# Performance work log

Measured on AMD Instinct MI355X. Metric: run time of the kernel, lower is better.

## Reference

```python
import jax, jax.numpy as jnp
import numpy as np

DIM = 128
HEADS = 8
DIM_HEAD = 128  # must equal DIM for the module's shapes to be consistent
INNER = HEADS * DIM_HEAD  # 1024
B, N = 16, 2048
SCALE = 1.0 / (DIM // 2 + 1)  # 1/65


def setup_inputs() -> dict:
    key = jax.random.key(0)
    k1, k2, k3 = jax.random.split(key, 3)
    x = jax.random.normal(k1, (B, N, DIM), dtype=jnp.float32)
    w_qkv = jax.random.normal(k2, (DIM, 3 * INNER), dtype=jnp.float32) * (DIM ** -0.5)
    w_out = jax.random.normal(k3, (INNER, DIM), dtype=jnp.float32) * (INNER ** -0.5)
    b_out = jnp.zeros((DIM,), dtype=jnp.float32)
    return {"x": x, "w_qkv": w_qkv, "w_out": w_out, "b_out": b_out}


def reference(x, w_qkv, w_out, b_out):
    b, n, dim = x.shape
    qkv = x @ w_qkv                                   # [b, n, 3*inner]
    q, k, v = jnp.split(qkv, 3, axis=-1)
    # b n (h d) -> b h n d
    to_heads = lambda t: t.reshape(b, n, HEADS, DIM_HEAD).transpose(0, 2, 1, 3)
    q, k, v = to_heads(q), to_heads(k), to_heads(v)
    xq_ft = jnp.abs(jnp.fft.rfft(q * SCALE, axis=-1))  # [b, h, n, f] real
    xk_ft = jnp.abs(jnp.fft.rfft(k * SCALE, axis=-1))
    xv_ft = jnp.fft.rfft(v, axis=-1)                   # complex
    att = jnp.einsum('bhex,bhey->bhxy', xq_ft, xk_ft)  # [b, h, f, f]
    att = jax.nn.softmax(att, axis=-1)
    xqkv_ft = jnp.einsum('bhxy,bhey->bhex', att.astype(xv_ft.dtype), xv_ft)
    out = jnp.fft.irfft(xqkv_ft, n=dim, axis=-1)       # [b, h, n, dim]
    out = out.transpose(0, 2, 1, 3).reshape(b, n, HEADS * dim)  # b n (h d)
    return out @ w_out + b_out
```

## Files before the change

### kernel.cpp

```cpp
#include <hip/hip_runtime.h>
#include <hip/hip_bf16.h>
#include <math.h>

#define NB    16
#define NSEQ  2048
#define MROWS (NB*NSEQ)
#define QKT_ROWS 1088

typedef __attribute__((ext_vector_type(8))) short bf16x8;
typedef __attribute__((ext_vector_type(4))) float f32x4;

__device__ __forceinline__ void g2l16(const void* g, void* l) {
    __builtin_amdgcn_global_load_lds(
        (const __attribute__((address_space(1))) void*)g,
        (__attribute__((address_space(3))) void*)l, 16, 0, 0);
}

__device__ __forceinline__ ushort f2bfu(float x) {
    __hip_bfloat16 t = __float2bfloat16(x);
    return *reinterpret_cast<ushort*>(&t);
}

__global__ __launch_bounds__(256) void k_misc(const float* __restrict__ x,
                                              const float* __restrict__ wqkv,
                                              const float* __restrict__ wout,
                                              __hip_bfloat16* __restrict__ Xb,
                                              ushort* __restrict__ Wvb,
                                              ushort* __restrict__ Wqkb,
                                              ushort* __restrict__ Gcat,
                                              ushort* __restrict__ Fcs,
                                              ushort* __restrict__ Bas) {
    __shared__ float tc[128], ts[128];
    int tid = threadIdx.x;
    int bid = blockIdx.x;
    if (bid < 4096) {
        int i = bid * 256 + tid;
        float4 v = ((const float4*)x)[i];
        __hip_bfloat16 o[4] = {__float2bfloat16(v.x), __float2bfloat16(v.y),
                               __float2bfloat16(v.z), __float2bfloat16(v.w)};
        *(ushort4*)((ushort*)Xb + (size_t)i * 4) = *(const ushort4*)o;
    } else if (bid < 4224) {
        int u = bid - 4096;
        float4 v = *(const float4*)(wqkv + (size_t)u * 3072 + 2048 + tid * 4);
        ushort o[4] = {f2bfu(v.x), f2bfu(v.y), f2bfu(v.z), f2bfu(v.w)};
        *(ushort4*)(Wvb + (size_t)u * 1024 + tid * 4) = *(const ushort4*)o;
    } else if (bid < 4352) {
        int u = bid - 4224;
        #pragma unroll
        for (int it = 0; it < 2; ++it) {
            int i = it * 256 + tid;
            float4 v = ((const float4*)(wqkv + (size_t)u * 3072))[i];
            ushort o[4] = {f2bfu(v.x), f2bfu(v.y), f2bfu(v.z), f2bfu(v.w)};
            *(ushort4*)(Wqkb + (size_t)u * 2048 + i * 4) = *(const ushort4*)o;
        }
    } else if (bid < 4872) {
        int hx = bid - 4352;
        if (tid < 128) {
            float a = (float)tid / 64.0f;
            tc[tid] = cospif(a);
            ts[tid] = sinpif(a);
        }
        __syncthreads();
        if (tid < 128) {
            int h = hx / 65, xx = hx - h * 65;
            float w = (xx == 0 || xx == 64) ? (1.0f / 128.0f) : (2.0f / 128.0f);
            float ar = 0.f, ai = 0.f;
            #pragma unroll 8
            for (int d = 0; d < 128; ++d) {
                float wv = wout[(size_t)(h * 128 + d) * 128 + tid];
                int m = (xx * d) & 127;
                ar = fmaf(wv, tc[m], ar);
                ai = fmaf(wv, ts[m], ai);
            }
            ushort* gp = Gcat + ((size_t)(h * 128 + tid)) * 160;
            gp[xx] = f2bfu(ar * w);
            gp[80 + xx] = f2bfu(-ai * w);
            if (xx == 0) {
                for (int k = 65; k < 80; ++k) gp[k] = 0;
                for (int k = 145; k < 160; ++k) gp[k] = 0;
            }
        }
    } else if (bid < 4888) {
        int r = (bid - 4872) * 16 + (tid >> 4);
        int d = r & 127;
        int y0 = (tid & 15) * 6;
        #pragma unroll
        for (int k = 0; k < 6; ++k) {
            int y = y0 + k;
            float v = 0.f;
            if (y < 65) {
                float a = (float)((d * y) & 127) / 64.0f;
                v = (r < 128) ? cospif(a) : -sinpif(a);
            }
            Fcs[r * 96 + y] = f2bfu(v);
        }
    } else {
        int idx = bid - 4888;
        int rj = idx * 16 + (tid >> 4);
        int ri = (rj >= 80) ? 1 : 0;
        int f = rj - ri * 80;
        int d0 = (tid & 15) * 8;
        #pragma unroll
        for (int k = 0; k < 8; ++k) {
            int d = d0 + k;
            float a = (float)((f * d) & 127) / 64.0f;
            float v = (ri ? -sinpif(a) : cospif(a)) * (1.0f / 65.0f);
            Bas[rj * 128 + d] = f2bfu(v);
        }
    }
}

__global__ __launch_bounds__(256) void k_wfold(const ushort* __restrict__ Wqkb,
                                               const ushort* __restrict__ Bas,
                                               ushort* __restrict__ Wt2) {
    __shared__ ushort As[128 * 128];
    __shared__ ushort Bs[160 * 128];
    int tid = threadIdx.x;
    int wave = tid >> 6, lane = tid & 63;
    int reg = blockIdx.x >> 3, h = blockIdx.x & 7;
    const ushort* ga = Wqkb + reg * 1024 + h * 128;
    #pragma unroll
    for (int it = 0; it < 8; ++it) {
        int q0 = wave * 512 + it * 64;
        int q = q0 + lane;
        int row = q >> 4, cp = q & 15;
        int gc = cp ^ (row & 15);
        g2l16(ga + (size_t)row * 2048 + gc * 8, As + q0 * 8);
    }
    #pragma unroll
    for (int it = 0; it < 10; ++it) {
        int q0 = it * 256 + wave * 64;
        int q = q0 + lane;
        int row = q >> 4, cp = q & 15;
        int gc = cp ^ (row & 15);
        g2l16(Bas + (size_t)row * 128 + gc * 8, Bs + q0 * 8);
    }
    __syncthreads();

    f32x4 acc[4][5];
    #pragma unroll
    for (int i = 0; i < 4; ++i)
        #pragma unroll
        for (int j = 0; j < 5; ++j) acc[i][j] = (f32x4){0.f, 0.f, 0.f, 0.f};

    int lr = lane & 15, lk = lane >> 4;
    int wr = (wave >> 1) * 64;
    int wn = (wave & 1) * 80;
    #pragma unroll
    for (int kk = 0; kk < 4; ++kk) {
        bf16x8 af[4], bfr[5];
        int c = kk * 4 + lk;
        #pragma unroll
        for (int i = 0; i < 4; ++i) {
            int m = wr + i * 16 + lr;
            af[i] = *(const bf16x8*)(As + m * 128 + (c ^ (m & 15)) * 8);
        }
        #pragma unroll
        for (int j = 0; j < 5; ++j) {
            int n = wn + j * 16 + lr;
            bfr[j] = *(const bf16x8*)(Bs + n * 128 + (c ^ (n & 15)) * 8);
        }
        #pragma unroll
        for (int i = 0; i < 4; ++i)
            #pragma unroll
            for (int j = 0; j < 5; ++j)
                acc[i][j] = __builtin_amdgcn_mfma_f32_16x16x32_bf16(af[i], bfr[j], acc[i][j], 0, 0, 0);
    }

    #pragma unroll
    for (int j = 0; j < 5; ++j) {
        int rj = wn + j * 16 + lr;
        int n = (h * 2 + reg) * 160 + rj;
        #pragma unroll
        for (int i = 0; i < 4; ++i) {
            int c0 = wr + i * 16 + lk * 4;
            union { ushort4 u4; ushort u[4]; } pk;
            #pragma unroll
            for (int r = 0; r < 4; ++r) pk.u[r] = f2bfu(acc[i][j][r]);
            *(ushort4*)(Wt2 + (size_t)n * 128 + c0) = pk.u4;
        }
    }
}

__global__ __launch_bounds__(256, 1) void k_fuse(const __hip_bfloat16* __restrict__ Xb,
                                                 const ushort* __restrict__ Wt2,
                                                 float* __restrict__ attp) {
    __shared__ ushort Bs[320 * 128];
    __shared__ ushort As[128 * 128];
    __shared__ ushort S[160 * 128];
    int tid = threadIdx.x;
    int wave = tid >> 6, lane = tid & 63;
    int lr = lane & 15, lk = lane >> 4;
    int lin = blockIdx.y * 128 + blockIdx.x;
    int nl = (lin & 7) * 128 + (lin >> 3);
    int b = nl >> 6;
    int rem = nl & 63;
    int h = rem >> 3, ech = rem & 7;
    size_t erow0 = (size_t)b * NSEQ + (size_t)ech * 256;

    const ushort* wh = Wt2 + (size_t)h * 320 * 128;
    #pragma unroll
    for (int it = 0; it < 20; ++it) {
        int q0 = it * 256 + wave * 64;
        int q = q0 + lane;
        int row = q >> 4, cp = q & 15;
        int gc = cp ^ (row & 15);
        g2l16(wh + (size_t)row * 128 + gc * 8, Bs + q0 * 8);
    }
    {
        const ushort* gx = (const ushort*)Xb + erow0 * 128;
        #pragma unroll
        for (int it = 0; it < 8; ++it) {
            int q0 = wave * 512 + it * 64;
            int q = q0 + lane;
            int row = q >> 4, cp = q & 15;
            int gc = cp ^ (row & 15);
            g2l16(gx + (size_t)row * 128 + gc * 8, As + q0 * 8);
        }
    }
    __syncthreads();

    f32x4 acc2a[5], acc2b[5];
    #pragma unroll
    for (int j = 0; j < 5; ++j) {
        acc2a[j] = (f32x4){0.f, 0.f, 0.f, 0.f};
        acc2b[j] = (f32x4){0.f, 0.f, 0.f, 0.f};
    }

    int esl = wave * 32;
    #pragma unroll
    for (int et = 0; et < 2; ++et) {
        f32x4 acc1[20][2];
        #pragma unroll
        for (int nt = 0; nt < 20; ++nt)
            #pragma unroll
            for (int ei = 0; ei < 2; ++ei) acc1[nt][ei] = (f32x4){0.f, 0.f, 0.f, 0.f};
        #pragma unroll
        for (int ks = 0; ks < 4; ++ks) {
            int c = ks * 4 + lk;
            bf16x8 xa[2];
            #pragma unroll
            for (int ei = 0; ei < 2; ++ei) {
                int m = esl + ei * 16 + lr;
                xa[ei] = *(const bf16x8*)(As + m * 128 + (c ^ (m & 15)) * 8);
            }
            #pragma unroll
            for (int nt = 0; nt < 20; ++nt) {
                int n = nt * 16 + lr;
                bf16x8 wb = *(const bf16x8*)(Bs + n * 128 + (c ^ (n & 15)) * 8);
                #pragma unroll
                for (int ei = 0; ei < 2; ++ei)
                    acc1[nt][ei] = __builtin_amdgcn_mfma_f32_16x16x32_bf16(xa[ei], wb, acc1[nt][ei], 0, 0, 0);
            }
        }
        #pragma unroll
        for (int grp = 0; grp < 2; ++grp) {
            #pragma unroll
            for (int t = 0; t < 5; ++t) {
                int srow = grp * 80 + t * 16 + lr;
                int sw = (srow & 7) << 3;
                #pragma unroll
                for (int ei = 0; ei < 2; ++ei) {
                    f32x4 re = acc1[grp * 10 + t][ei];
                    f32x4 im = acc1[grp * 10 + t + 5][ei];
                    union { ushort4 u4; ushort u[4]; } pk;
                    #pragma unroll
                    for (int r = 0; r < 4; ++r)
                        pk.u[r] = f2bfu(__builtin_amdgcn_sqrtf(re[r] * re[r] + im[r] * im[r]));
                    int e4 = (esl + ei * 16 + lk * 4) ^ sw;
                    *(ushort4*)(S + srow * 128 + e4) = pk.u4;
                }
            }
        }
        __syncthreads();
        if (et == 0) {
            const ushort* gx = (const ushort*)Xb + (erow0 + 128) * 128;
            #pragma unroll
            for (int it = 0; it < 8; ++it) {
                int q0 = wave * 512 + it * 64;
                int q = q0 + lane;
                int row = q >> 4, cp = q & 15;
                int gc = cp ^ (row & 15);
                g2l16(gx + (size_t)row * 128 + gc * 8, As + q0 * 8);
            }
        }
        #pragma unroll
        for (int ks = 0; ks < 4; ++ks) {
            int cg = ks * 4 + lk;
            int xr = wave * 16 + lr;
            bf16x8 qa = *(const bf16x8*)(S + xr * 128 + ((cg ^ (xr & 7)) * 8));
            bf16x8 qb;
            if (wave == 0) {
                int xr2 = 64 + lr;
                qb = *(const bf16x8*)(S + xr2 * 128 + ((cg ^ (xr2 & 7)) * 8));
            }
            #pragma unroll
            for (int ty = 0; ty < 5; ++ty) {
                int yr = 80 + ty * 16 + lr;
                bf16x8 kb = *(const bf16x8*)(S + yr * 128 + ((cg ^ (yr & 7)) * 8));
                acc2a[ty] = __builtin_amdgcn_mfma_f32_16x16x32_bf16(qa, kb, acc2a[ty], 0, 0, 0);
                if (wave == 0)
                    acc2b[ty] = __builtin_amdgcn_mfma_f32_16x16x32_bf16(qb, kb, acc2b[ty], 0, 0, 0);
            }
        }
        if (et == 0) __syncthreads();
    }

    float* outp = attp + ((size_t)(b * 8 + h) * 8 + ech) * 6400;
    #pragma unroll
    for (int ty = 0; ty < 5; ++ty) {
        #pragma unroll
        for (int r = 0; r < 4; ++r) {
            outp[(wave * 16 + lk * 4 + r) * 80 + ty * 16 + lr] = acc2a[ty][r];
            if (wave == 0)
                outp[(64 + lk * 4 + r) * 80 + ty * 16 + lr] = acc2b[ty][r];
        }
    }
}

__global__ void k_softmax(const float* __restrict__ attp, ushort* __restrict__ AttB) {
    int xx = blockIdx.x;
    int bh = blockIdx.y;
    int lane = threadIdx.x;
    ushort* Ab = AttB + (size_t)bh * 8320;
    if (xx >= 65) {
        Ab[xx * 104 + lane] = 0;
        if (lane < 40) Ab[xx * 104 + 64 + lane] = 0;
        return;
    }
    const float* base = attp + (size_t)bh * 8 * 6400 + xx * 80;
    float v0 = 0.f, v1 = 0.f;
    #pragma unroll
    for (int c = 0; c < 8; ++c) {
        v0 += base[(size_t)c * 6400 + lane];
        if (lane == 0) v1 += base[(size_t)c * 6400 + 64];
    }
    float v1b = __shfl(v1, 0);
    float m = fmaxf(v0, v1b);
    #pragma unroll
    for (int off = 32; off >= 1; off >>= 1) m = fmaxf(m, __shfl_xor(m, off));
    float e0 = expf(v0 - m);
    float e1 = expf(v1b - m);
    float s = e0;
    #pragma unroll
    for (int off = 32; off >= 1; off >>= 1) s += __shfl_xor(s, off);
    s += e1;
    float inv = 1.0f / s;
    Ab[xx * 104 + lane] = f2bfu(e0 * inv);
    if (lane == 0) Ab[xx * 104 + 64] = f2bfu(e1 * inv);
    if (lane < 39) Ab[xx * 104 + 65 + lane] = 0;
}

__global__ __launch_bounds__(256) void k_TP(const ushort* __restrict__ AttB,
                                            const ushort* __restrict__ Fcs,
                                            const ushort* __restrict__ Gcat,
                                            ushort* __restrict__ Pt) {
    __shared__ ushort A3[128 * 168];
    int tid = threadIdx.x;
    int wave = tid >> 6, lane = tid & 63;
    int lr = lane & 15, quad = lane >> 4;
    int chalf = blockIdx.x, bh = blockIdx.y;
    int b = bh >> 3, h = bh & 7;

    uint2 z2; z2.x = 0; z2.y = 0;
    uint2* A3v = (uint2*)A3;
    #pragma unroll 4
    for (int i = tid; i < 128 * 168 / 4; i += 256) A3v[i] = z2;
    __syncthreads();
    const ushort* Ab = AttB + (size_t)bh * 8320;

    f32x4 acc1[4][5];
    #pragma unroll
    for (int i = 0; i < 4; ++i)
        #pragma unroll
        for (int j = 0; j < 5; ++j) acc1[i][j] = (f32x4){0.f, 0.f, 0.f, 0.f};
    #pragma unroll
    for (int ks = 0; ks < 3; ++ks) {
        bf16x8 af[4], bfr[5];
        #pragma unroll
        for (int mi = 0; mi < 4; ++mi)
            af[mi] = *(const bf16x8*)(Fcs + (size_t)((wave * 4 + mi) * 16 + lr) * 96 + ks * 32 + quad * 8);
        #pragma unroll
        for (int nt = 0; nt < 5; ++nt)
            bfr[nt] = *(const bf16x8*)(Ab + (nt * 16 + lr) * 104 + ks * 32 + quad * 8);
        #pragma unroll
        for (int mi = 0; mi < 4; ++mi)
            #pragma unroll
            for (int nt = 0; nt < 5; ++nt)
                acc1[mi][nt] = __builtin_amdgcn_mfma_f32_16x16x32_bf16(af[mi], bfr[nt], acc1[mi][nt], 0, 0, 0);
    }
    #pragma unroll
    for (int nt = 0; nt < 5; ++nt) {
        int x = nt * 16 + lr;
        if (x < 65) {
            #pragma unroll
            for (int mi = 0; mi < 4; ++mi) {
                int wbase = (wave * 4 + mi) * 16 + quad * 4;
                #pragma unroll
                for (int r = 0; r < 4; ++r) {
                    int which = wbase + r;
                    int d = which & 127;
                    int kc = (which >> 7) * 80 + x;
                    A3[d * 168 + kc] = f2bfu(acc1[mi][nt][r]);
                }
            }
        }
    }
    __syncthreads();

    f32x4 acc2[2][4];
    #pragma unroll
    for (int i = 0; i < 2; ++i)
        #pragma unroll
        for (int j = 0; j < 4; ++j) acc2[i][j] = (f32x4){0.f, 0.f, 0.f, 0.f};
    const ushort* Gh = Gcat + (size_t)h * 128 * 160;
    #pragma unroll
    for (int ks = 0; ks < 5; ++ks) {
        bf16x8 a2[2], b2[4];
        #pragma unroll
        for (int mi = 0; mi < 2; ++mi)
            a2[mi] = *(const bf16x8*)(A3 + ((wave * 2 + mi) * 16 + lr) * 168 + ks * 32 + quad * 8);
        #pragma unroll
        for (int nt = 0; nt < 4; ++nt)
            b2[nt] = *(const bf16x8*)(Gh + (size_t)(chalf * 64 + nt * 16 + lr) * 160 + ks * 32 + quad * 8);
        #pragma unroll
        for (int mi = 0; mi < 2; ++mi)
            #pragma unroll
            for (int nt = 0; nt < 4; ++nt)
                acc2[mi][nt] = __builtin_amdgcn_mfma_f32_16x16x32_bf16(a2[mi], b2[nt], acc2[mi][nt], 0, 0, 0);
    }
    #pragma unroll
    for (int mi = 0; mi < 2; ++mi) {
        int dbase = (wave * 2 + mi) * 16 + quad * 4;
        #pragma unroll
        for (int nt = 0; nt < 4; ++nt) {
            int c = chalf * 64 + nt * 16 + lr;
            union { ushort4 u4; ushort u[4]; } pk;
            #pragma unroll
            for (int r = 0; r < 4; ++r) pk.u[r] = f2bfu(acc2[mi][nt][r]);
            *(ushort4*)(Pt + ((size_t)(b * 128 + c)) * 1024 + h * 128 + dbase) = pk.u4;
        }
    }
}

__global__ __launch_bounds__(256) void k_R(const ushort* __restrict__ Wvb,
                                           const ushort* __restrict__ Pt,
                                           ushort* __restrict__ Rt) {
    __shared__ ushort As[128 * 128];
    __shared__ ushort Bs[128 * 128];
    int tid = threadIdx.x;
    int wave = tid >> 6, lane = tid & 63;
    int b = blockIdx.x;
    const ushort* pb = Pt + (size_t)b * 128 * 1024;

    f32x4 acc[4][4];
    #pragma unroll
    for (int i = 0; i < 4; ++i)
        #pragma unroll
        for (int j = 0; j < 4; ++j) acc[i][j] = (f32x4){0.f, 0.f, 0.f, 0.f};

    int lr = lane & 15, lk = lane >> 4;
    int wr = (wave >> 1) * 64, wc = (wave & 1) * 64;

    for (int k0 = 0; k0 < 1024; k0 += 128) {
        __syncthreads();
        #pragma unroll
        for (int it = 0; it < 8; ++it) {
            int q = wave * 512 + it * 64 + lane;
            int row = q >> 4, cp = q & 15;
            int gc = cp ^ (row & 15);
            int lbase = (wave * 512 + it * 64) * 8;
            g2l16(Wvb + (size_t)row * 1024 + k0 + gc * 8, As + lbase);
            g2l16(pb + (size_t)row * 1024 + k0 + gc * 8, Bs + lbase);
        }
        __syncthreads();
        #pragma unroll
        for (int kk = 0; kk < 4; ++kk) {
            bf16x8 af[4], bfr[4];
            int c = kk * 4 + lk;
            #pragma unroll
            for (int i = 0; i < 4; ++i) {
                int m = wr + i * 16 + lr;
                af[i] = *(const bf16x8*)(As + m * 128 + (c ^ (m & 15)) * 8);
                int n = wc + i * 16 + lr;
                bfr[i] = *(const bf16x8*)(Bs + n * 128 + (c ^ (n & 15)) * 8);
            }
            #pragma unroll
            for (int i = 0; i < 4; ++i)
                #pragma unroll
                for (int j = 0; j < 4; ++j)
                    acc[i][j] = __builtin_amdgcn_mfma_f32_16x16x32_bf16(af[i], bfr[j], acc[i][j], 0, 0, 0);
        }
    }
    #pragma unroll
    for (int i = 0; i < 4; ++i) {
        int ubase = wr + i * 16 + lk * 4;
        #pragma unroll
        for (int j = 0; j < 4; ++j) {
            int n = wc + j * 16 + lr;
            union { ushort4 u4; ushort u[4]; } pk;
            #pragma unroll
            for (int r = 0; r < 4; ++r) pk.u[r] = f2bfu(acc[i][j][r]);
            *(ushort4*)(Rt + (size_t)b * 16384 + n * 128 + ubase) = pk.u4;
        }
    }
}

__global__ __launch_bounds__(256) void k_out(const __hip_bfloat16* __restrict__ Xb,
                                             const ushort* __restrict__ Rt,
                                             const float* __restrict__ bout,
                                             float* __restrict__ out) {
    __shared__ ushort As[128 * 128];
    __shared__ ushort Bs[128 * 128];
    int tid = threadIdx.x;
    int wave = tid >> 6, lane = tid & 63;
    int m0 = blockIdx.x * 128;
    int b = blockIdx.x >> 4;
    const ushort* ga = (const ushort*)Xb + (size_t)m0 * 128;
    const ushort* gb = Rt + (size_t)b * 16384;
    #pragma unroll
    for (int it = 0; it < 8; ++it) {
        int q = wave * 512 + it * 64 + lane;
        int row = q >> 4, cp = q & 15;
        int gc = cp ^ (row & 15);
        int lbase = (wave * 512 + it * 64) * 8;
        g2l16(ga + (size_t)row * 128 + gc * 8, As + lbase);
        g2l16(gb + (size_t)row * 128 + gc * 8, Bs + lbase);
    }
    __syncthreads();

    f32x4 acc[4][4];
    #pragma unroll
    for (int i = 0; i < 4; ++i)
        #pragma unroll
        for (int j = 0; j < 4; ++j) acc[i][j] = (f32x4){0.f, 0.f, 0.f, 0.f};

    int lr = lane & 15, lk = lane >> 4;
    int wr = (wave >> 1) * 64, wc = (wave & 1) * 64;
    #pragma unroll
    for (int kk = 0; kk < 4; ++kk) {
        bf16x8 af[4], bfr[4];
        int c = kk * 4 + lk;
        #pragma unroll
        for (int i = 0; i < 4; ++i) {
            int m = wr + i * 16 + lr;
            af[i] = *(const bf16x8*)(As + m * 128 + (c ^ (m & 15)) * 8);
            int n = wc + i * 16 + lr;
            bfr[i] = *(const bf16x8*)(Bs + n * 128 + (c ^ (n & 15)) * 8);
        }
        #pragma unroll
        for (int i = 0; i < 4; ++i)
            #pragma unroll
            for (int j = 0; j < 4; ++j)
                acc[i][j] = __builtin_amdgcn_mfma_f32_16x16x32_bf16(af[i], bfr[j], acc[i][j], 0, 0, 0);
    }

    #pragma unroll
    for (int i = 0; i < 4; ++i) {
        int gr = m0 + wr + i * 16 + lk * 4;
        #pragma unroll
        for (int j = 0; j < 4; ++j) {
            int gcol = wc + j * 16 + lr;
            float bias = bout[gcol];
            #pragma unroll
            for (int r = 0; r < 4; ++r)
                out[(size_t)(gr + r) * 128 + gcol] = acc[i][j][r] + bias;
        }
    }
}

extern "C" void kernel_launch(void* const* d_in, const int* in_sizes, int n_in,
                              void* d_out, int out_size, void* d_ws, size_t ws_size,
                              hipStream_t stream) {
    const float* x    = (const float*)d_in[0];
    const float* wqkv = (const float*)d_in[1];
    const float* wout = (const float*)d_in[2];
    const float* bout = (const float*)d_in[3];
    float* out = (float*)d_out;

    char* ws = (char*)d_ws;
    size_t off = 0;
    auto alloc = [&](size_t bytes) -> void* {
        void* p = (void*)(ws + off);
        off += (bytes + 255) & ~(size_t)255;
        return p;
    };
    ushort* Wt2  = (ushort*)alloc((size_t)8 * 320 * 128 * 2);
    ushort* Gcat = (ushort*)alloc((size_t)8 * 128 * 160 * 2);
    ushort* Fcs  = (ushort*)alloc((size_t)256 * 96 * 2);
    ushort* Wvb  = (ushort*)alloc((size_t)128 * 1024 * 2);
    ushort* Wqkb = (ushort*)alloc((size_t)128 * 2048 * 2);
    ushort* Bas  = (ushort*)alloc((size_t)160 * 128 * 2);
    __hip_bfloat16* Xb = (__hip_bfloat16*)alloc((size_t)MROWS * 128 * 2);
    float* attp = (float*)alloc((size_t)128 * 8 * 6400 * 4);
    ushort* AttB = (ushort*)alloc((size_t)128 * 8320 * 2);
    ushort* Pt  = (ushort*)alloc((size_t)16 * 128 * 1024 * 2);
    ushort* Rt  = (ushort*)alloc((size_t)16 * 128 * 128 * 2);

    k_misc<<<dim3(4898), 256, 0, stream>>>(x, wqkv, wout, Xb, Wvb, Wqkb, Gcat, Fcs, Bas);
    k_wfold<<<dim3(16), 256, 0, stream>>>(Wqkb, Bas, Wt2);
    k_fuse<<<dim3(128, 8), 256, 0, stream>>>(Xb, Wt2, attp);
    k_softmax<<<dim3(80, 128), 64, 0, stream>>>(attp, AttB);
    k_TP<<<dim3(2, 128), 256, 0, stream>>>(AttB, Fcs, Gcat, Pt);
    k_R<<<dim3(16), 256, 0, stream>>>(Wvb, Pt, Rt);
    k_out<<<dim3(256), 256, 0, stream>>>(Xb, Rt, bout, out);
}
```

Before: 171.0 us.

## Restructure fused QK-spectrum kernel with register-resident weights and larger sequence chunks

```diff
diff --git a/kernel.cpp b/kernel.cpp
--- a/kernel.cpp
+++ b/kernel.cpp
@@ -5,7 +5,6 @@
 #define NB    16
 #define NSEQ  2048
 #define MROWS (NB*NSEQ)
-#define QKT_ROWS 1088
 
 typedef __attribute__((ext_vector_type(8))) short bf16x8;
 typedef __attribute__((ext_vector_type(4))) float f32x4;
@@ -182,37 +181,34 @@
     }
 }
 
-__global__ __launch_bounds__(256, 1) void k_fuse(const __hip_bfloat16* __restrict__ Xb,
+__global__ __launch_bounds__(320, 3) void k_fuse(const __hip_bfloat16* __restrict__ Xb,
                                                  const ushort* __restrict__ Wt2,
                                                  float* __restrict__ attp) {
-    __shared__ ushort Bs[320 * 128];
     __shared__ ushort As[128 * 128];
     __shared__ ushort S[160 * 128];
     int tid = threadIdx.x;
     int wave = tid >> 6, lane = tid & 63;
     int lr = lane & 15, lk = lane >> 4;
     int lin = blockIdx.y * 128 + blockIdx.x;
-    int nl = (lin & 7) * 128 + (lin >> 3);
-    int b = nl >> 6;
-    int rem = nl & 63;
-    int h = rem >> 3, ech = rem & 7;
-    size_t erow0 = (size_t)b * NSEQ + (size_t)ech * 256;
-
+    int nl = (lin & 7) * 64 + (lin >> 3);
+    int b = nl >> 5;
+    int epart = (nl >> 3) & 3, h = nl & 7;
+    size_t erow0 = (size_t)b * NSEQ + (size_t)epart * 512;
     const ushort* wh = Wt2 + (size_t)h * 320 * 128;
-    #pragma unroll
-    for (int it = 0; it < 20; ++it) {
-        int q0 = it * 256 + wave * 64;
-        int q = q0 + lane;
-        int row = q >> 4, cp = q & 15;
-        int gc = cp ^ (row & 15);
-        g2l16(wh + (size_t)row * 128 + gc * 8, Bs + q0 * 8);
-    }
+
+    bf16x8 bw[4][4];
+    #pragma unroll
+    for (int ks = 0; ks < 4; ++ks)
+        #pragma unroll
+        for (int rb = 0; rb < 4; ++rb) {
+            int n = rb * 80 + wave * 16 + lr;
+            bw[ks][rb] = *(const bf16x8*)(wh + (size_t)n * 128 + (ks * 4 + lk) * 8);
+        }
+
     {
         const ushort* gx = (const ushort*)Xb + erow0 * 128;
-        #pragma unroll
-        for (int it = 0; it < 8; ++it) {
-            int q0 = wave * 512 + it * 64;
-            int q = q0 + lane;
+        for (int r = wave; r < 32; r += 5) {
+            int q0 = r * 64, q = q0 + lane;
             int row = q >> 4, cp = q & 15;
             int gc = cp ^ (row & 15);
             g2l16(gx + (size_t)row * 128 + gc * 8, As + q0 * 8);
@@ -220,65 +216,42 @@
     }
     __syncthreads();
 
-    f32x4 acc2a[5], acc2b[5];
-    #pragma unroll
-    for (int j = 0; j < 5; ++j) {
-        acc2a[j] = (f32x4){0.f, 0.f, 0.f, 0.f};
-        acc2b[j] = (f32x4){0.f, 0.f, 0.f, 0.f};
-    }
-
-    int esl = wave * 32;
-    #pragma unroll
-    for (int et = 0; et < 2; ++et) {
-        f32x4 acc1[20][2];
-        #pragma unroll
-        for (int nt = 0; nt < 20; ++nt)
-            #pragma unroll
-            for (int ei = 0; ei < 2; ++ei) acc1[nt][ei] = (f32x4){0.f, 0.f, 0.f, 0.f};
-        #pragma unroll
-        for (int ks = 0; ks < 4; ++ks) {
-            int c = ks * 4 + lk;
-            bf16x8 xa[2];
-            #pragma unroll
-            for (int ei = 0; ei < 2; ++ei) {
-                int m = esl + ei * 16 + lr;
-                xa[ei] = *(const bf16x8*)(As + m * 128 + (c ^ (m & 15)) * 8);
-            }
-            #pragma unroll
-            for (int nt = 0; nt < 20; ++nt) {
-                int n = nt * 16 + lr;
-                bf16x8 wb = *(const bf16x8*)(Bs + n * 128 + (c ^ (n & 15)) * 8);
+    f32x4 acc2[5];
+    #pragma unroll
+    for (int j = 0; j < 5; ++j) acc2[j] = (f32x4){0.f, 0.f, 0.f, 0.f};
+
+    for (int it = 0; it < 4; ++it) {
+        #pragma unroll
+        for (int et = 0; et < 8; ++et) {
+            f32x4 a4[4];
+            #pragma unroll
+            for (int rb = 0; rb < 4; ++rb) a4[rb] = (f32x4){0.f, 0.f, 0.f, 0.f};
+            #pragma unroll
+            for (int ks = 0; ks < 4; ++ks) {
+                int m = et * 16 + lr;
+                bf16x8 xa = *(const bf16x8*)(As + m * 128 + (((ks * 4 + lk) ^ (m & 15))) * 8);
                 #pragma unroll
-                for (int ei = 0; ei < 2; ++ei)
-                    acc1[nt][ei] = __builtin_amdgcn_mfma_f32_16x16x32_bf16(xa[ei], wb, acc1[nt][ei], 0, 0, 0);
-            }
-        }
-        #pragma unroll
-        for (int grp = 0; grp < 2; ++grp) {
-            #pragma unroll
-            for (int t = 0; t < 5; ++t) {
-                int srow = grp * 80 + t * 16 + lr;
-                int sw = (srow & 7) << 3;
-                #pragma unroll
-                for (int ei = 0; ei < 2; ++ei) {
-                    f32x4 re = acc1[grp * 10 + t][ei];
-                    f32x4 im = acc1[grp * 10 + t + 5][ei];
-                    union { ushort4 u4; ushort u[4]; } pk;
-                    #pragma unroll
-                    for (int r = 0; r < 4; ++r)
-                        pk.u[r] = f2bfu(__builtin_amdgcn_sqrtf(re[r] * re[r] + im[r] * im[r]));
-                    int e4 = (esl + ei * 16 + lk * 4) ^ sw;
-                    *(ushort4*)(S + srow * 128 + e4) = pk.u4;
-                }
-            }
+                for (int rb = 0; rb < 4; ++rb)
+                    a4[rb] = __builtin_amdgcn_mfma_f32_16x16x32_bf16(xa, bw[ks][rb], a4[rb], 0, 0, 0);
+            }
+            int e4 = et * 16 + lk * 4;
+            int cq = e4 >> 3, sub = e4 & 7;
+            union { ushort4 u4; ushort u[4]; } pq, pk2;
+            #pragma unroll
+            for (int r = 0; r < 4; ++r) {
+                pq.u[r]  = f2bfu(__builtin_amdgcn_sqrtf(a4[0][r] * a4[0][r] + a4[1][r] * a4[1][r]));
+                pk2.u[r] = f2bfu(__builtin_amdgcn_sqrtf(a4[2][r] * a4[2][r] + a4[3][r] * a4[3][r]));
+            }
+            int fq = wave * 16 + lr;
+            int fk = 80 + wave * 16 + lr;
+            *(ushort4*)(S + fq * 128 + ((cq ^ (fq & 15)) << 3) + sub) = pq.u4;
+            *(ushort4*)(S + fk * 128 + ((cq ^ (fk & 15)) << 3) + sub) = pk2.u4;
         }
         __syncthreads();
-        if (et == 0) {
-            const ushort* gx = (const ushort*)Xb + (erow0 + 128) * 128;
-            #pragma unroll
-            for (int it = 0; it < 8; ++it) {
-                int q0 = wave * 512 + it * 64;
-                int q = q0 + lane;
+        if (it < 3) {
+            const ushort* gx = (const ushort*)Xb + (erow0 + (size_t)(it + 1) * 128) * 128;
+            for (int r = wave; r < 32; r += 5) {
+                int q0 = r * 64, q = q0 + lane;
                 int row = q >> 4, cp = q & 15;
                 int gc = cp ^ (row & 15);
                 g2l16(gx + (size_t)row * 128 + gc * 8, As + q0 * 8);
@@ -288,34 +261,23 @@
         for (int ks = 0; ks < 4; ++ks) {
             int cg = ks * 4 + lk;
             int xr = wave * 16 + lr;
-            bf16x8 qa = *(const bf16x8*)(S + xr * 128 + ((cg ^ (xr & 7)) * 8));
-            bf16x8 qb;
-            if (wave == 0) {
-                int xr2 = 64 + lr;
-                qb = *(const bf16x8*)(S + xr2 * 128 + ((cg ^ (xr2 & 7)) * 8));
-            }
-            #pragma unroll
-            for (int ty = 0; ty < 5; ++ty) {
-                int yr = 80 + ty * 16 + lr;
-                bf16x8 kb = *(const bf16x8*)(S + yr * 128 + ((cg ^ (yr & 7)) * 8));
-                acc2a[ty] = __builtin_amdgcn_mfma_f32_16x16x32_bf16(qa, kb, acc2a[ty], 0, 0, 0);
-                if (wave == 0)
-                    acc2b[ty] = __builtin_amdgcn_mfma_f32_16x16x32_bf16(qb, kb, acc2b[ty], 0, 0, 0);
-            }
-        }
-        if (et == 0) __syncthreads();
-    }
-
-    float* outp = attp + ((size_t)(b * 8 + h) * 8 + ech) * 6400;
-    #pragma unroll
-    for (int ty = 0; ty < 5; ++ty) {
-        #pragma unroll
-        for (int r = 0; r < 4; ++r) {
-            outp[(wave * 16 + lk * 4 + r) * 80 + ty * 16 + lr] = acc2a[ty][r];
-            if (wave == 0)
-                outp[(64 + lk * 4 + r) * 80 + ty * 16 + lr] = acc2b[ty][r];
-        }
-    }
+            bf16x8 qa = *(const bf16x8*)(S + xr * 128 + ((cg ^ (xr & 15)) << 3));
+            #pragma unroll
+            for (int kt = 0; kt < 5; ++kt) {
+                int yr = 80 + kt * 16 + lr;
+                bf16x8 kb = *(const bf16x8*)(S + yr * 128 + ((cg ^ (yr & 15)) << 3));
+                acc2[kt] = __builtin_amdgcn_mfma_f32_16x16x32_bf16(qa, kb, acc2[kt], 0, 0, 0);
+            }
+        }
+        __syncthreads();
+    }
+
+    float* outp = attp + ((size_t)(b * 8 + h) * 4 + epart) * 6400;
+    #pragma unroll
+    for (int kt = 0; kt < 5; ++kt)
+        #pragma unroll
+        for (int r = 0; r < 4; ++r)
+            outp[(wave * 16 + lk * 4 + r) * 80 + kt * 16 + lr] = acc2[kt][r];
 }
 
 __global__ void k_softmax(const float* __restrict__ attp, ushort* __restrict__ AttB) {
@@ -328,10 +290,10 @@
         if (lane < 40) Ab[xx * 104 + 64 + lane] = 0;
         return;
     }
-    const float* base = attp + (size_t)bh * 8 * 6400 + xx * 80;
+    const float* base = attp + (size_t)bh * 4 * 6400 + xx * 80;
     float v0 = 0.f, v1 = 0.f;
     #pragma unroll
-    for (int c = 0; c < 8; ++c) {
+    for (int c = 0; c < 4; ++c) {
         v0 += base[(size_t)c * 6400 + lane];
         if (lane == 0) v1 += base[(size_t)c * 6400 + 64];
     }
@@ -592,14 +554,14 @@
     ushort* Wqkb = (ushort*)alloc((size_t)128 * 2048 * 2);
     ushort* Bas  = (ushort*)alloc((size_t)160 * 128 * 2);
     __hip_bfloat16* Xb = (__hip_bfloat16*)alloc((size_t)MROWS * 128 * 2);
-    float* attp = (float*)alloc((size_t)128 * 8 * 6400 * 4);
+    float* attp = (float*)alloc((size_t)128 * 4 * 6400 * 4);
     ushort* AttB = (ushort*)alloc((size_t)128 * 8320 * 2);
     ushort* Pt  = (ushort*)alloc((size_t)16 * 128 * 1024 * 2);
     ushort* Rt  = (ushort*)alloc((size_t)16 * 128 * 128 * 2);
 
     k_misc<<<dim3(4898), 256, 0, stream>>>(x, wqkv, wout, Xb, Wvb, Wqkb, Gcat, Fcs, Bas);
     k_wfold<<<dim3(16), 256, 0, stream>>>(Wqkb, Bas, Wt2);
-    k_fuse<<<dim3(128, 8), 256, 0, stream>>>(Xb, Wt2, attp);
+    k_fuse<<<dim3(128, 4), 320, 0, stream>>>(Xb, Wt2, attp);
     k_softmax<<<dim3(80, 128), 64, 0, stream>>>(attp, AttB);
     k_TP<<<dim3(2, 128), 256, 0, stream>>>(AttB, Fcs, Gcat, Pt);
     k_R<<<dim3(16), 256, 0, stream>>>(Wvb, Pt, Rt);
```

Result: faster. 159.1 us (-7.0%).
